# Optimization experiments

Measured on AMD Instinct MI355X. Metric: run time of the kernel, lower is better.

The kernel has to match this reference:

```python
import jax, jax.numpy as jnp
import numpy as np

N_EMBD = 256
BLOCK_SIZE = 128
N_HEAD = 8
HEAD_SIZE = 256
B = 256
T = 128


def setup_inputs() -> dict:
    key = jax.random.key(0)
    ks = jax.random.split(key, 9)
    s = 0.02
    return {
        "x": jax.random.normal(ks[0], (B, T, N_EMBD), dtype=jnp.float32),
        # torch Linear weight layout: [out_features, in_features], stacked over heads
        "Wq": jax.random.normal(ks[1], (N_HEAD, HEAD_SIZE, N_EMBD), dtype=jnp.float32) * s,
        "bq": jax.random.normal(ks[2], (N_HEAD, HEAD_SIZE), dtype=jnp.float32) * s,
        "Wk": jax.random.normal(ks[3], (N_HEAD, HEAD_SIZE, N_EMBD), dtype=jnp.float32) * s,
        "bk": jax.random.normal(ks[4], (N_HEAD, HEAD_SIZE), dtype=jnp.float32) * s,
        "Wv": jax.random.normal(ks[5], (N_HEAD, HEAD_SIZE, N_EMBD), dtype=jnp.float32) * s,
        "bv": jax.random.normal(ks[6], (N_HEAD, HEAD_SIZE), dtype=jnp.float32) * s,
        "Wp": jax.random.normal(ks[7], (N_EMBD, N_EMBD), dtype=jnp.float32) * s,
        "bp": jax.random.normal(ks[8], (N_EMBD,), dtype=jnp.float32) * s,
    }


def reference(x, Wq, bq, Wk, bk, Wv, bv, Wp, bp):
    Bb, Tt, C = x.shape
    scale = C ** (-0.5)  # NOTE: original scales by n_embd (input C), not head_size
    # per-head projections: [h, b, t, d]
    q = jnp.einsum("btc,hdc->hbtd", x, Wq) + bq[:, None, None, :]
    k = jnp.einsum("btc,hdc->hbtd", x, Wk) + bk[:, None, None, :]
    v = jnp.einsum("btc,hdc->hbtd", x, Wv) + bv[:, None, None, :]
    att = jnp.einsum("hbtd,hbsd->hbts", q, k) * scale  # [h,b,t,s]
    causal = jnp.tril(jnp.ones((Tt, Tt), dtype=bool))
    att = jnp.where(causal, att, -jnp.inf)
    att = jax.nn.softmax(att, axis=-1)
    out = jnp.einsum("hbts,hbsd->hbtd", att, v)
    # torch.cat along dim=0 (batch concat, as written in the source)
    out = out.reshape(out.shape[0] * Bb, Tt, out.shape[-1])  # [h*b, t, head_size]
    return out @ Wp.T + bp
```

## Files before the change

### kernel.cpp

```cpp
#include <hip/hip_runtime.h>
#include <hip/hip_bf16.h>
#include <stdint.h>


#define TT 128

typedef __attribute__((ext_vector_type(8))) short short8;
typedef __attribute__((ext_vector_type(4))) float f32x4;

#define WS_X    0u
#define WS_M    16777216u
#define WS_WM   17825792u
#define WS_WB   18874368u
#define WS_BB   18939904u
#define WS_CQ   18948096u

#define LX     0
#define LT     65536
#define LP     65536
#define LH     98304
#define R_UV   131072
#define R_RED  132096
#define LDS_SIZE 134144

#define VMCNT0() asm volatile("s_waitcnt vmcnt(0)" ::: "memory")
#define LGKM0()  asm volatile("s_waitcnt lgkmcnt(0)" ::: "memory")
#define BAR()    do { asm volatile("" ::: "memory"); __builtin_amdgcn_s_barrier(); asm volatile("" ::: "memory"); } while (0)
#define PRIO1()  __builtin_amdgcn_s_setprio(1)
#define PRIO0()  __builtin_amdgcn_s_setprio(0)

typedef __attribute__((address_space(3))) uint32_t lds_u32;
typedef __attribute__((address_space(1))) const uint32_t glb_u32;

__device__ __forceinline__ unsigned short f2bf(float x) {
    union { float f; unsigned u; } v; v.f = x;
    unsigned r = v.u + 0x7FFFu + ((v.u >> 16) & 1u);
    return (unsigned short)(r >> 16);
}
__device__ __forceinline__ unsigned pk2(float a, float b) {
    return (unsigned)f2bf(a) | ((unsigned)f2bf(b) << 16);
}

__global__ __launch_bounds__(256) void convert_pre(
    const float* __restrict__ x,
    const float* __restrict__ Wq, const float* __restrict__ bq,
    const float* __restrict__ Wk, const float* __restrict__ bk,
    const float* __restrict__ Wv, const float* __restrict__ bv,
    const float* __restrict__ Wp, const float* __restrict__ bp,
    char* __restrict__ ws)
{
    extern __shared__ char clds[];
    const int tid = threadIdx.x;
    const int bid = blockIdx.x;

    if (bid < 256) {
        const float* src = x + (size_t)bid * 32768;
        char* dst = ws + WS_X + (size_t)bid * 65536;
        for (int i = tid; i < 8192; i += 256) {
            float4 v = ((const float4*)src)[i];
            int row = i >> 6, c4 = i & 63;
            uint2 u; u.x = pk2(v.x, v.y); u.y = pk2(v.z, v.w);
            *(uint2*)(clds + row * 512 + ((c4 * 8) ^ ((row & 7) << 4))) = u;
        }
        __syncthreads();
        for (int i = tid; i < 4096; i += 256) {
            int l = i & 63, ks = (i >> 6) & 7, g = i >> 9;
            int r = g * 16 + (l & 15);
            int boff = ks * 64 + (l >> 4) * 16;
            uint4 q = *(const uint4*)(clds + r * 512 + (boff ^ ((r & 7) << 4)));
            ((uint4*)dst)[i] = q;
        }
        return;
    }
    if (bid < 384) {
        int id = bid - 256, h = id >> 4, st = id & 15;
        float* wkL = (float*)clds;
        for (int i = tid; i < 4096; i += 256) {
            int d = i >> 4, cc = i & 15;
            wkL[i] = Wk[(size_t)h * 65536 + d * 256 + st * 16 + cc];
        }
        __syncthreads();
        const int c = tid;
        float acc[16];
        #pragma unroll
        for (int j = 0; j < 16; ++j) acc[j] = 0.f;
        #pragma unroll 4
        for (int d = 0; d < 256; ++d) {
            float a = Wq[(size_t)h * 65536 + d * 256 + c];
            #pragma unroll
            for (int j = 0; j < 16; ++j) acc[j] += a * wkL[d * 16 + j];
        }
        char* base = ws + WS_M + (size_t)h * 131072;
        int ks = c >> 5, lgp = (c >> 3) & 3, jb = c & 7;
        #pragma unroll
        for (int j = 0; j < 16; ++j) {
            int cp = st * 16 + j;
            *(unsigned short*)(base + (((st * 8 + ks)) << 10)
                + ((cp & 15) + 16 * lgp) * 16 + jb * 2) = f2bf(acc[j] * 0.0625f);
        }
        return;
    }
    if (bid < 512) {
        int id = bid - 384, h = id >> 4, st = id & 15;
        float* wpL = (float*)clds;
        for (int i = tid; i < 4096; i += 256) {
            int e = i >> 8, d = i & 255;
            wpL[e * 257 + d] = Wp[(size_t)(st * 16 + e) * 256 + d];
        }
        __syncthreads();
        const int c = tid;
        float acc[16];
        #pragma unroll
        for (int j = 0; j < 16; ++j) acc[j] = 0.f;
        #pragma unroll 4
        for (int d = 0; d < 256; ++d) {
            float wv = Wv[(size_t)h * 65536 + d * 256 + c];
            #pragma unroll
            for (int j = 0; j < 16; ++j) acc[j] += wv * wpL[j * 257 + d];
        }
        char* base = ws + WS_WM + (size_t)h * 131072;
        int ks = c >> 5, lgp = (c >> 3) & 3, jb = c & 7;
        #pragma unroll
        for (int j = 0; j < 16; ++j) {
            *(unsigned short*)(base + (((st * 8 + ks)) << 10)
                + (j + 16 * lgp) * 16 + jb * 2) = f2bf(acc[j]);
        }
        return;
    }
    if (bid < 520) {
        const int h = bid - 512;
        {
            uint4 z = {0u,0u,0u,0u};
            for (int i = tid; i < 512; i += 256)
                ((uint4*)(ws + WS_WB + (size_t)h * 8192))[i] = z;
        }
        float* tK = (float*)clds;
        float* tQ = (float*)(clds + 16384);
        const int c = tid;
        float s1 = 0.f, s2 = 0.f;
        for (int d0 = 0; d0 < 256; d0 += 16) {
            __syncthreads();
            for (int i = tid; i < 1024; i += 256) {
                int row = i >> 6, c4 = i & 63;
                ((float4*)tK)[row * 64 + c4] =
                    ((const float4*)(Wk + (size_t)h * 65536 + (size_t)(d0 + row) * 256))[c4];
                ((float4*)tQ)[row * 64 + c4] =
                    ((const float4*)(Wq + (size_t)h * 65536 + (size_t)(d0 + row) * 256))[c4];
            }
            __syncthreads();
            #pragma unroll
            for (int dd = 0; dd < 16; ++dd) {
                s1 += tK[dd * 256 + c] * bq[h * 256 + d0 + dd];
                s2 += tQ[dd * 256 + c] * bk[h * 256 + d0 + dd];
            }
        }
        int ks = c >> 5, lgp = (c >> 3) & 3, jb = c & 7;
        char* base = ws + WS_WB + (size_t)h * 8192 + ks * 1024;
        *(unsigned short*)(base + (0 + 16 * lgp) * 16 + jb * 2) = f2bf(s2 * 0.0625f);
        *(unsigned short*)(base + (1 + 16 * lgp) * 16 + jb * 2) = f2bf(s1 * 0.0625f);
        float* red = (float*)(clds + 32768);
        red[tid] = bq[h * 256 + tid] * bk[h * 256 + tid];
        __syncthreads();
        if (tid == 0) {
            float cq = 0.f;
            for (int d = 0; d < 256; ++d) cq += red[d];
            *(float*)(ws + WS_CQ + h * 4) = cq * 0.0625f;
        }
        return;
    }
    {
        const int st = bid - 520;
        float* wpT = (float*)clds;
        float* bvL = (float*)(clds + 17408);
        for (int i = tid; i < 1024; i += 256) {
            int row = i >> 6, c4 = i & 63;
            float4 v = ((const float4*)(Wp + (size_t)(st * 16 + row) * 256))[c4];
            float* dstp = wpT + row * 257 + c4 * 4;
            dstp[0] = v.x; dstp[1] = v.y; dstp[2] = v.z; dstp[3] = v.w;
        }
        for (int i = tid; i < 512; i += 256)
            ((float4*)bvL)[i] = ((const float4*)bv)[i];
        __syncthreads();
        const int el = tid >> 4, dg = tid & 15;
        #pragma unroll
        for (int h = 0; h < 8; ++h) {
            float p = 0.f;
            #pragma unroll
            for (int dd = 0; dd < 16; ++dd) {
                int d = dg * 16 + dd;
                p += bvL[h * 256 + d] * wpT[el * 257 + d];
            }
            p += __shfl_xor(p, 1);
            p += __shfl_xor(p, 2);
            p += __shfl_xor(p, 4);
            p += __shfl_xor(p, 8);
            if (dg == 0)
                *(float*)(ws + WS_BB + (size_t)h * 1024 + (st * 16 + el) * 4)
                    = bp[st * 16 + el] + p;
        }
        return;
    }
}

__global__ __launch_bounds__(512, 1) void mha_fused(
    const char* __restrict__ ws, float* __restrict__ out)
{
    extern __shared__ char lds[];
    const int tid = threadIdx.x;
    const int w  = tid >> 6, l = tid & 63;
    const int lg = l >> 4, lr = l & 15;
    const int mq = w & 3, nh = w >> 2;
    const int bid = blockIdx.x;
    const int xcd = bid & 7, j = bid >> 3;
    const int h = j & 7;
    const int b = ((j >> 3) << 3) | xcd;
    const size_t orow = ((size_t)(h * 256 + b)) * TT;

    const char* Xf  = ws + WS_X  + (size_t)b * 65536;
    const char* Mh  = ws + WS_M  + (size_t)h * 131072;
    const char* WMh = ws + WS_WM + (size_t)h * 131072;
    const char* WBh = ws + WS_WB + (size_t)h * 8192;

    {
        const char* src = Xf + tid * 16;
        #pragma unroll
        for (int p = 0; p < 8; ++p)
            __builtin_amdgcn_global_load_lds((glb_u32*)(src + p * 8192),
                (lds_u32*)(lds + LX + tid * 16 + p * 8192), 16, 0, 0);
    }
    VMCNT0(); BAR();

    {
        f32x4 vacc[2] = {f32x4{0.f,0.f,0.f,0.f}, f32x4{0.f,0.f,0.f,0.f}};
        #pragma unroll
        for (int ks = 0; ks < 8; ++ks) {
            short8 wb  = *(const short8*)(WBh + (ks << 10) + l*16);
            short8 xa0 = *(const short8*)(lds + LX + (((mq*2 + 0)*8 + ks) << 10) + l*16);
            short8 xa1 = *(const short8*)(lds + LX + (((mq*2 + 1)*8 + ks) << 10) + l*16);
            vacc[0] = __builtin_amdgcn_mfma_f32_16x16x32_bf16(xa0, wb, vacc[0], 0, 0, 0);
            vacc[1] = __builtin_amdgcn_mfma_f32_16x16x32_bf16(xa1, wb, vacc[1], 0, 0, 0);
        }
        if (nh == 0 && lr < 2) {
            #pragma unroll
            for (int mt = 0; mt < 2; ++mt)
                #pragma unroll
                for (int r = 0; r < 4; ++r) {
                    int t = mq*32 + mt*16 + lg*4 + r;
                    *(float*)(lds + R_UV + lr*512 + t*4) = vacc[mt][r];
                }
        }
    }

    #pragma unroll
    for (int pass = 0; pass < 2; ++pass) {
        const int ga = w*2 + pass;
        f32x4 acc[8];
        #pragma unroll
        for (int i = 0; i < 8; ++i) acc[i] = f32x4{0.f,0.f,0.f,0.f};
        #pragma unroll
        for (int ks = 0; ks < 8; ++ks) {
            short8 nb = *(const short8*)(Mh + (((ga*8 + ks)) << 10) + l*16);
            PRIO1();
            #pragma unroll
            for (int mt = 0; mt < 8; ++mt) {
                short8 xa = *(const short8*)(lds + LX + (((mt*8 + ks)) << 10) + l*16);
                acc[mt] = __builtin_amdgcn_mfma_f32_16x16x32_bf16(xa, nb, acc[mt], 0, 0, 0);
            }
            PRIO0();
        }
        #pragma unroll
        for (int mt = 0; mt < 8; ++mt)
            #pragma unroll
            for (int r = 0; r < 4; ++r) {
                int t = mt*16 + lg*4 + r;
                int c = ga*16 + lr;
                *(unsigned short*)(lds + LT + t*512 + ((c*2) ^ ((t&7)<<4)))
                    = f2bf(acc[mt][r]);
            }
    }
    LGKM0(); BAR();

    f32x4 sacc[2][4];
    #pragma unroll
    for (int i = 0; i < 2; ++i)
        #pragma unroll
        for (int jj = 0; jj < 4; ++jj) sacc[i][jj] = f32x4{0.f,0.f,0.f,0.f};
    #pragma unroll
    for (int ks2 = 0; ks2 < 8; ++ks2) {
        short8 ta[2];
        #pragma unroll
        for (int mt = 0; mt < 2; ++mt) {
            int t2 = mq*32 + mt*16 + lr;
            ta[mt] = *(const short8*)(lds + LT + t2*512 + ((ks2*64 + lg*16) ^ ((t2&7)<<4)));
        }
        short8 sb[4];
        #pragma unroll
        for (int nt = 0; nt < 4; ++nt)
            sb[nt] = *(const short8*)(lds + LX + (((nh*4+nt)*8 + ks2) << 10) + l*16);
        PRIO1();
        #pragma unroll
        for (int mt = 0; mt < 2; ++mt)
            #pragma unroll
            for (int nt = 0; nt < 4; ++nt)
                sacc[mt][nt] = __builtin_amdgcn_mfma_f32_16x16x32_bf16(ta[mt], sb[nt], sacc[mt][nt], 0, 0, 0);
        PRIO0();
    }

    {
        const float cq = *(const float*)(ws + WS_CQ + h*4);
        float uu[4];
        #pragma unroll
        for (int nt = 0; nt < 4; ++nt)
            uu[nt] = *(const float*)(lds + R_UV + 512 + (nh*64 + nt*16 + lr)*4);
        float* redM = (float*)(lds + R_RED);
        float* redS = redM + 256;
        float rmax[2][4];
        #pragma unroll
        for (int mt = 0; mt < 2; ++mt)
            #pragma unroll
            for (int r = 0; r < 4; ++r) {
                int t = mq*32 + mt*16 + lg*4 + r;
                float vt = *(const float*)(lds + R_UV + t*4) + cq;
                float m = -1e30f;
                #pragma unroll
                for (int nt = 0; nt < 4; ++nt) {
                    int s = nh*64 + nt*16 + lr;
                    float sv = sacc[mt][nt][r] + vt + uu[nt];
                    if (s > t) sv = -1e30f;
                    sacc[mt][nt][r] = sv;
                    m = fmaxf(m, sv);
                }
                m = fmaxf(m, __shfl_xor(m, 1));
                m = fmaxf(m, __shfl_xor(m, 2));
                m = fmaxf(m, __shfl_xor(m, 4));
                m = fmaxf(m, __shfl_xor(m, 8));
                rmax[mt][r] = m;
            }
        if (lr == 0) {
            #pragma unroll
            for (int mt = 0; mt < 2; ++mt)
                #pragma unroll
                for (int r = 0; r < 4; ++r)
                    redM[nh*128 + mq*32 + mt*16 + lg*4 + r] = rmax[mt][r];
        }
        LGKM0(); BAR();
        float rsum[2][4];
        #pragma unroll
        for (int mt = 0; mt < 2; ++mt)
            #pragma unroll
            for (int r = 0; r < 4; ++r) {
                int t = mq*32 + mt*16 + lg*4 + r;
                float m = fmaxf(redM[t], redM[128 + t]);
                float ssum = 0.f;
                #pragma unroll
                for (int nt = 0; nt < 4; ++nt) {
                    float p = __expf(sacc[mt][nt][r] - m);
                    sacc[mt][nt][r] = p;
                    ssum += p;
                }
                ssum += __shfl_xor(ssum, 1);
                ssum += __shfl_xor(ssum, 2);
                ssum += __shfl_xor(ssum, 4);
                ssum += __shfl_xor(ssum, 8);
                rsum[mt][r] = ssum;
            }
        if (lr == 0) {
            #pragma unroll
            for (int mt = 0; mt < 2; ++mt)
                #pragma unroll
                for (int r = 0; r < 4; ++r)
                    redS[nh*128 + mq*32 + mt*16 + lg*4 + r] = rsum[mt][r];
        }
        LGKM0(); BAR();
        #pragma unroll
        for (int mt = 0; mt < 2; ++mt)
            #pragma unroll
            for (int r = 0; r < 4; ++r) {
                int t = mq*32 + mt*16 + lg*4 + r;
                float inv = 1.0f / (redS[t] + redS[128 + t]);
                #pragma unroll
                for (int nt = 0; nt < 4; ++nt) {
                    int s = nh*64 + nt*16 + lr;
                    *(unsigned short*)(lds + LP + t*256 + ((s*2) ^ ((t&7)<<4)))
                        = f2bf(sacc[mt][nt][r] * inv);
                }
            }
    }
    LGKM0(); BAR();

    short8 pa[2][4];
    #pragma unroll
    for (int mt = 0; mt < 2; ++mt) {
        int t2 = mq*32 + mt*16 + lr;
        #pragma unroll
        for (int ks = 0; ks < 4; ++ks)
            pa[mt][ks] = *(const short8*)(lds + LP + t2*256 + ((ks*64 + lg*16) ^ ((t2&7)<<4)));
    }

    const float* bbp = (const float*)(ws + WS_BB + h*1024);
    #pragma unroll
    for (int eh = 0; eh < 2; ++eh) {
        {
            f32x4 acc[8];
            #pragma unroll
            for (int i = 0; i < 8; ++i) acc[i] = f32x4{0.f,0.f,0.f,0.f};
            #pragma unroll
            for (int ks = 0; ks < 8; ++ks) {
                short8 wa = *(const short8*)(WMh + ((((eh*8 + w)*8 + ks)) << 10) + l*16);
                PRIO1();
                #pragma unroll
                for (int nt = 0; nt < 8; ++nt) {
                    short8 sb = *(const short8*)(lds + LX + (((nt*8 + ks)) << 10) + l*16);
                    acc[nt] = __builtin_amdgcn_mfma_f32_16x16x32_bf16(wa, sb, acc[nt], 0, 0, 0);
                }
                PRIO0();
            }
            #pragma unroll
            for (int nt = 0; nt < 8; ++nt)
                #pragma unroll
                for (int r = 0; r < 4; ++r) {
                    int el = w*16 + lg*4 + r;
                    int s  = nt*16 + lr;
                    *(unsigned short*)(lds + LH + el*256 + ((s*2) ^ ((el&7)<<4)))
                        = f2bf(acc[nt][r]);
                }
        }
        LGKM0(); BAR();
        #pragma unroll
        for (int ec = 0; ec < 2; ++ec) {
            f32x4 acc[2][2];
            #pragma unroll
            for (int i = 0; i < 2; ++i)
                #pragma unroll
                for (int jj = 0; jj < 2; ++jj) acc[i][jj] = f32x4{0.f,0.f,0.f,0.f};
            #pragma unroll
            for (int ks = 0; ks < 4; ++ks) {
                short8 hb[2];
                #pragma unroll
                for (int nt = 0; nt < 2; ++nt) {
                    int erl = (nh*4 + ec*2 + nt)*16 + lr;
                    hb[nt] = *(const short8*)(lds + LH + erl*256 + ((ks*64 + lg*16) ^ ((erl&7)<<4)));
                }
                PRIO1();
                #pragma unroll
                for (int mt = 0; mt < 2; ++mt)
                    #pragma unroll
                    for (int nt = 0; nt < 2; ++nt)
                        acc[mt][nt] = __builtin_amdgcn_mfma_f32_16x16x32_bf16(pa[mt][ks], hb[nt], acc[mt][nt], 0, 0, 0);
                PRIO0();
            }
            #pragma unroll
            for (int nt = 0; nt < 2; ++nt) {
                int e = eh*128 + (nh*4 + ec*2 + nt)*16 + lr;
                float bbv = bbp[e];
                #pragma unroll
                for (int mt = 0; mt < 2; ++mt)
                    #pragma unroll
                    for (int r = 0; r < 4; ++r) {
                        int t = mq*32 + mt*16 + lg*4 + r;
                        out[(orow + t) * 256 + e] = acc[mt][nt][r] + bbv;
                    }
            }
        }
        if (eh == 0) { LGKM0(); BAR(); }
    }
}

extern "C" void kernel_launch(void* const* d_in, const int* in_sizes, int n_in,
                              void* d_out, int out_size, void* d_ws, size_t ws_size,
                              hipStream_t stream) {
    (void)in_sizes; (void)n_in; (void)out_size; (void)ws_size;
    const float* x  = (const float*)d_in[0];
    const float* Wq = (const float*)d_in[1];
    const float* bq = (const float*)d_in[2];
    const float* Wk = (const float*)d_in[3];
    const float* bk = (const float*)d_in[4];
    const float* Wv = (const float*)d_in[5];
    const float* bv = (const float*)d_in[6];
    const float* Wp = (const float*)d_in[7];
    const float* bp = (const float*)d_in[8];
    char* ws = (char*)d_ws;

    hipFuncSetAttribute((const void*)convert_pre,
                        hipFuncAttributeMaxDynamicSharedMemorySize, 65536);
    convert_pre<<<dim3(536), dim3(256), 65536, stream>>>(
        x, Wq, bq, Wk, bk, Wv, bv, Wp, bp, ws);

    hipFuncSetAttribute((const void*)mha_fused,
                        hipFuncAttributeMaxDynamicSharedMemorySize, LDS_SIZE);
    mha_fused<<<dim3(2048), dim3(512), LDS_SIZE, stream>>>(ws, (float*)d_out);
}
```

Before: 267.2 us.

## Double workgroup to 1024 threads and repartition all GEMM stages across 16 waves

The fused attention kernel now runs 16 waves per block instead of 8, and every stage is repartitioned to match: the projection, scores, softmax, H and output GEMMs each handle half the tiles per wave. The goal is more latency hiding and more in-flight MFMA work per CU, since only one block of about 131 KB LDS fits per CU. The cost is more waves contending for the same LDS and barriers, less register reuse of loaded fragments per wave, and tighter register limits at 1024 threads.

```diff
diff --git a/kernel.cpp b/kernel.cpp
--- a/kernel.cpp
+++ b/kernel.cpp
@@ -202,14 +202,14 @@
     }
 }
 
-__global__ __launch_bounds__(512, 1) void mha_fused(
+__global__ __launch_bounds__(1024, 1) void mha_fused(
     const char* __restrict__ ws, float* __restrict__ out)
 {
     extern __shared__ char lds[];
     const int tid = threadIdx.x;
     const int w  = tid >> 6, l = tid & 63;
     const int lg = l >> 4, lr = l & 15;
-    const int mq = w & 3, nh = w >> 2;
+    const int mq = w & 7, nh = w >> 3;
     const int bid = blockIdx.x;
     const int xcd = bid & 7, j = bid >> 3;
     const int h = j & 7;
@@ -224,42 +224,36 @@
     {
         const char* src = Xf + tid * 16;
         #pragma unroll
-        for (int p = 0; p < 8; ++p)
-            __builtin_amdgcn_global_load_lds((glb_u32*)(src + p * 8192),
-                (lds_u32*)(lds + LX + tid * 16 + p * 8192), 16, 0, 0);
+        for (int p = 0; p < 4; ++p)
+            __builtin_amdgcn_global_load_lds((glb_u32*)(src + p * 16384),
+                (lds_u32*)(lds + LX + tid * 16 + p * 16384), 16, 0, 0);
     }
     VMCNT0(); BAR();
 
+    if (nh == 0) {
+        f32x4 vacc = f32x4{0.f,0.f,0.f,0.f};
+        #pragma unroll
+        for (int ks = 0; ks < 8; ++ks) {
+            short8 wb = *(const short8*)(WBh + (ks << 10) + l*16);
+            short8 xa = *(const short8*)(lds + LX + (((mq*8 + ks)) << 10) + l*16);
+            vacc = __builtin_amdgcn_mfma_f32_16x16x32_bf16(xa, wb, vacc, 0, 0, 0);
+        }
+        if (lr < 2) {
+            #pragma unroll
+            for (int r = 0; r < 4; ++r) {
+                int t = mq*16 + lg*4 + r;
+                *(float*)(lds + R_UV + lr*512 + t*4) = vacc[r];
+            }
+        }
+    }
+
     {
-        f32x4 vacc[2] = {f32x4{0.f,0.f,0.f,0.f}, f32x4{0.f,0.f,0.f,0.f}};
+        f32x4 acc[8];
+        #pragma unroll
+        for (int i = 0; i < 8; ++i) acc[i] = f32x4{0.f,0.f,0.f,0.f};
         #pragma unroll
         for (int ks = 0; ks < 8; ++ks) {
-            short8 wb  = *(const short8*)(WBh + (ks << 10) + l*16);
-            short8 xa0 = *(const short8*)(lds + LX + (((mq*2 + 0)*8 + ks) << 10) + l*16);
-            short8 xa1 = *(const short8*)(lds + LX + (((mq*2 + 1)*8 + ks) << 10) + l*16);
-            vacc[0] = __builtin_amdgcn_mfma_f32_16x16x32_bf16(xa0, wb, vacc[0], 0, 0, 0);
-            vacc[1] = __builtin_amdgcn_mfma_f32_16x16x32_bf16(xa1, wb, vacc[1], 0, 0, 0);
-        }
-        if (nh == 0 && lr < 2) {
-            #pragma unroll
-            for (int mt = 0; mt < 2; ++mt)
-                #pragma unroll
-                for (int r = 0; r < 4; ++r) {
-                    int t = mq*32 + mt*16 + lg*4 + r;
-                    *(float*)(lds + R_UV + lr*512 + t*4) = vacc[mt][r];
-                }
-        }
-    }
-
-    #pragma unroll
-    for (int pass = 0; pass < 2; ++pass) {
-        const int ga = w*2 + pass;
-        f32x4 acc[8];
-        #pragma unroll
-        for (int i = 0; i < 8; ++i) acc[i] = f32x4{0.f,0.f,0.f,0.f};
-        #pragma unroll
-        for (int ks = 0; ks < 8; ++ks) {
-            short8 nb = *(const short8*)(Mh + (((ga*8 + ks)) << 10) + l*16);
+            short8 nb = *(const short8*)(Mh + (((w*8 + ks)) << 10) + l*16);
             PRIO1();
             #pragma unroll
             for (int mt = 0; mt < 8; ++mt) {
@@ -273,36 +267,28 @@
             #pragma unroll
             for (int r = 0; r < 4; ++r) {
                 int t = mt*16 + lg*4 + r;
-                int c = ga*16 + lr;
+                int c = w*16 + lr;
                 *(unsigned short*)(lds + LT + t*512 + ((c*2) ^ ((t&7)<<4)))
                     = f2bf(acc[mt][r]);
             }
     }
     LGKM0(); BAR();
 
-    f32x4 sacc[2][4];
+    f32x4 sacc[4];
     #pragma unroll
-    for (int i = 0; i < 2; ++i)
-        #pragma unroll
-        for (int jj = 0; jj < 4; ++jj) sacc[i][jj] = f32x4{0.f,0.f,0.f,0.f};
+    for (int i = 0; i < 4; ++i) sacc[i] = f32x4{0.f,0.f,0.f,0.f};
     #pragma unroll
     for (int ks2 = 0; ks2 < 8; ++ks2) {
-        short8 ta[2];
-        #pragma unroll
-        for (int mt = 0; mt < 2; ++mt) {
-            int t2 = mq*32 + mt*16 + lr;
-            ta[mt] = *(const short8*)(lds + LT + t2*512 + ((ks2*64 + lg*16) ^ ((t2&7)<<4)));
-        }
+        int t2 = mq*16 + lr;
+        short8 ta = *(const short8*)(lds + LT + t2*512 + ((ks2*64 + lg*16) ^ ((t2&7)<<4)));
         short8 sb[4];
         #pragma unroll
         for (int nt = 0; nt < 4; ++nt)
             sb[nt] = *(const short8*)(lds + LX + (((nh*4+nt)*8 + ks2) << 10) + l*16);
         PRIO1();
         #pragma unroll
-        for (int mt = 0; mt < 2; ++mt)
-            #pragma unroll
-            for (int nt = 0; nt < 4; ++nt)
-                sacc[mt][nt] = __builtin_amdgcn_mfma_f32_16x16x32_bf16(ta[mt], sb[nt], sacc[mt][nt], 0, 0, 0);
+        for (int nt = 0; nt < 4; ++nt)
+            sacc[nt] = __builtin_amdgcn_mfma_f32_16x16x32_bf16(ta, sb[nt], sacc[nt], 0, 0, 0);
         PRIO0();
     }
 
@@ -314,113 +300,102 @@
             uu[nt] = *(const float*)(lds + R_UV + 512 + (nh*64 + nt*16 + lr)*4);
         float* redM = (float*)(lds + R_RED);
         float* redS = redM + 256;
-        float rmax[2][4];
-        #pragma unroll
-        for (int mt = 0; mt < 2; ++mt)
-            #pragma unroll
-            for (int r = 0; r < 4; ++r) {
-                int t = mq*32 + mt*16 + lg*4 + r;
-                float vt = *(const float*)(lds + R_UV + t*4) + cq;
-                float m = -1e30f;
-                #pragma unroll
-                for (int nt = 0; nt < 4; ++nt) {
-                    int s = nh*64 + nt*16 + lr;
-                    float sv = sacc[mt][nt][r] + vt + uu[nt];
-                    if (s > t) sv = -1e30f;
-                    sacc[mt][nt][r] = sv;
-                    m = fmaxf(m, sv);
-                }
-                m = fmaxf(m, __shfl_xor(m, 1));
-                m = fmaxf(m, __shfl_xor(m, 2));
-                m = fmaxf(m, __shfl_xor(m, 4));
-                m = fmaxf(m, __shfl_xor(m, 8));
-                rmax[mt][r] = m;
-            }
+        float rmax[4];
+        #pragma unroll
+        for (int r = 0; r < 4; ++r) {
+            int t = mq*16 + lg*4 + r;
+            float vt = *(const float*)(lds + R_UV + t*4) + cq;
+            float m = -1e30f;
+            #pragma unroll
+            for (int nt = 0; nt < 4; ++nt) {
+                int s = nh*64 + nt*16 + lr;
+                float sv = sacc[nt][r] + vt + uu[nt];
+                if (s > t) sv = -1e30f;
+                sacc[nt][r] = sv;
+                m = fmaxf(m, sv);
+            }
+            m = fmaxf(m, __shfl_xor(m, 1));
+            m = fmaxf(m, __shfl_xor(m, 2));
+            m = fmaxf(m, __shfl_xor(m, 4));
+            m = fmaxf(m, __shfl_xor(m, 8));
+            rmax[r] = m;
+        }
         if (lr == 0) {
             #pragma unroll
-            for (int mt = 0; mt < 2; ++mt)
-                #pragma unroll
-                for (int r = 0; r < 4; ++r)
-                    redM[nh*128 + mq*32 + mt*16 + lg*4 + r] = rmax[mt][r];
+            for (int r = 0; r < 4; ++r)
+                redM[nh*128 + mq*16 + lg*4 + r] = rmax[r];
         }
         LGKM0(); BAR();
-        float rsum[2][4];
-        #pragma unroll
-        for (int mt = 0; mt < 2; ++mt)
-            #pragma unroll
-            for (int r = 0; r < 4; ++r) {
-                int t = mq*32 + mt*16 + lg*4 + r;
-                float m = fmaxf(redM[t], redM[128 + t]);
-                float ssum = 0.f;
-                #pragma unroll
-                for (int nt = 0; nt < 4; ++nt) {
-                    float p = __expf(sacc[mt][nt][r] - m);
-                    sacc[mt][nt][r] = p;
-                    ssum += p;
-                }
-                ssum += __shfl_xor(ssum, 1);
-                ssum += __shfl_xor(ssum, 2);
-                ssum += __shfl_xor(ssum, 4);
-                ssum += __shfl_xor(ssum, 8);
-                rsum[mt][r] = ssum;
-            }
+        float rsum[4];
+        #pragma unroll
+        for (int r = 0; r < 4; ++r) {
+            int t = mq*16 + lg*4 + r;
+            float m = fmaxf(redM[t], redM[128 + t]);
+            float ssum = 0.f;
+            #pragma unroll
+            for (int nt = 0; nt < 4; ++nt) {
+                float p = __expf(sacc[nt][r] - m);
+                sacc[nt][r] = p;
+                ssum += p;
+            }
+            ssum += __shfl_xor(ssum, 1);
+            ssum += __shfl_xor(ssum, 2);
+            ssum += __shfl_xor(ssum, 4);
+            ssum += __shfl_xor(ssum, 8);
+            rsum[r] = ssum;
+        }
         if (lr == 0) {
             #pragma unroll
-            for (int mt = 0; mt < 2; ++mt)
-                #pragma unroll
-                for (int r = 0; r < 4; ++r)
-                    redS[nh*128 + mq*32 + mt*16 + lg*4 + r] = rsum[mt][r];
+            for (int r = 0; r < 4; ++r)
+                redS[nh*128 + mq*16 + lg*4 + r] = rsum[r];
         }
         LGKM0(); BAR();
         #pragma unroll
-        for (int mt = 0; mt < 2; ++mt)
-            #pragma unroll
-            for (int r = 0; r < 4; ++r) {
-                int t = mq*32 + mt*16 + lg*4 + r;
-                float inv = 1.0f / (redS[t] + redS[128 + t]);
-                #pragma unroll
-                for (int nt = 0; nt < 4; ++nt) {
-                    int s = nh*64 + nt*16 + lr;
-                    *(unsigned short*)(lds + LP + t*256 + ((s*2) ^ ((t&7)<<4)))
-                        = f2bf(sacc[mt][nt][r] * inv);
-                }
-            }
+        for (int r = 0; r < 4; ++r) {
+            int t = mq*16 + lg*4 + r;
+            float inv = 1.0f / (redS[t] + redS[128 + t]);
+            #pragma unroll
+            for (int nt = 0; nt < 4; ++nt) {
+                int s = nh*64 + nt*16 + lr;
+                *(unsigned short*)(lds + LP + t*256 + ((s*2) ^ ((t&7)<<4)))
+                    = f2bf(sacc[nt][r] * inv);
+            }
+        }
     }
     LGKM0(); BAR();
 
-    short8 pa[2][4];
-    #pragma unroll
-    for (int mt = 0; mt < 2; ++mt) {
-        int t2 = mq*32 + mt*16 + lr;
+    short8 pa[4];
+    {
+        int t2 = mq*16 + lr;
         #pragma unroll
         for (int ks = 0; ks < 4; ++ks)
-            pa[mt][ks] = *(const short8*)(lds + LP + t2*256 + ((ks*64 + lg*16) ^ ((t2&7)<<4)));
+            pa[ks] = *(const short8*)(lds + LP + t2*256 + ((ks*64 + lg*16) ^ ((t2&7)<<4)));
     }
 
     const float* bbp = (const float*)(ws + WS_BB + h*1024);
     #pragma unroll
     for (int eh = 0; eh < 2; ++eh) {
         {
-            f32x4 acc[8];
-            #pragma unroll
-            for (int i = 0; i < 8; ++i) acc[i] = f32x4{0.f,0.f,0.f,0.f};
+            f32x4 acc[4];
+            #pragma unroll
+            for (int i = 0; i < 4; ++i) acc[i] = f32x4{0.f,0.f,0.f,0.f};
             #pragma unroll
             for (int ks = 0; ks < 8; ++ks) {
-                short8 wa = *(const short8*)(WMh + ((((eh*8 + w)*8 + ks)) << 10) + l*16);
+                short8 wa = *(const short8*)(WMh + ((((eh*8 + mq)*8 + ks)) << 10) + l*16);
                 PRIO1();
                 #pragma unroll
-                for (int nt = 0; nt < 8; ++nt) {
-                    short8 sb = *(const short8*)(lds + LX + (((nt*8 + ks)) << 10) + l*16);
+                for (int nt = 0; nt < 4; ++nt) {
+                    short8 sb = *(const short8*)(lds + LX + ((((nh*4+nt)*8 + ks)) << 10) + l*16);
                     acc[nt] = __builtin_amdgcn_mfma_f32_16x16x32_bf16(wa, sb, acc[nt], 0, 0, 0);
                 }
                 PRIO0();
             }
             #pragma unroll
-            for (int nt = 0; nt < 8; ++nt)
+            for (int nt = 0; nt < 4; ++nt)
                 #pragma unroll
                 for (int r = 0; r < 4; ++r) {
-                    int el = w*16 + lg*4 + r;
-                    int s  = nt*16 + lr;
+                    int el = mq*16 + lg*4 + r;
+                    int s  = (nh*4+nt)*16 + lr;
                     *(unsigned short*)(lds + LH + el*256 + ((s*2) ^ ((el&7)<<4)))
                         = f2bf(acc[nt][r]);
                 }
@@ -428,38 +403,32 @@
         LGKM0(); BAR();
         #pragma unroll
         for (int ec = 0; ec < 2; ++ec) {
-            f32x4 acc[2][2];
-            #pragma unroll
-            for (int i = 0; i < 2; ++i)
-                #pragma unroll
-                for (int jj = 0; jj < 2; ++jj) acc[i][jj] = f32x4{0.f,0.f,0.f,0.f};
+            f32x4 acc[2];
+            acc[0] = f32x4{0.f,0.f,0.f,0.f};
+            acc[1] = f32x4{0.f,0.f,0.f,0.f};
             #pragma unroll
             for (int ks = 0; ks < 4; ++ks) {
                 short8 hb[2];
                 #pragma unroll
                 for (int nt = 0; nt < 2; ++nt) {
-                    int erl = (nh*4 + ec*2 + nt)*16 + lr;
+                    int erl = nh*64 + (ec*2 + nt)*16 + lr;
                     hb[nt] = *(const short8*)(lds + LH + erl*256 + ((ks*64 + lg*16) ^ ((erl&7)<<4)));
                 }
                 PRIO1();
                 #pragma unroll
-                for (int mt = 0; mt < 2; ++mt)
-                    #pragma unroll
-                    for (int nt = 0; nt < 2; ++nt)
-                        acc[mt][nt] = __builtin_amdgcn_mfma_f32_16x16x32_bf16(pa[mt][ks], hb[nt], acc[mt][nt], 0, 0, 0);
+                for (int nt = 0; nt < 2; ++nt)
+                    acc[nt] = __builtin_amdgcn_mfma_f32_16x16x32_bf16(pa[ks], hb[nt], acc[nt], 0, 0, 0);
                 PRIO0();
             }
             #pragma unroll
             for (int nt = 0; nt < 2; ++nt) {
-                int e = eh*128 + (nh*4 + ec*2 + nt)*16 + lr;
+                int e = eh*128 + nh*64 + (ec*2 + nt)*16 + lr;
                 float bbv = bbp[e];
                 #pragma unroll
-                for (int mt = 0; mt < 2; ++mt)
-                    #pragma unroll
-                    for (int r = 0; r < 4; ++r) {
-                        int t = mq*32 + mt*16 + lg*4 + r;
-                        out[(orow + t) * 256 + e] = acc[mt][nt][r] + bbv;
-                    }
+                for (int r = 0; r < 4; ++r) {
+                    int t = mq*16 + lg*4 + r;
+                    out[(orow + t) * 256 + e] = acc[nt][r] + bbv;
+                }
             }
         }
         if (eh == 0) { LGKM0(); BAR(); }
@@ -488,5 +457,5 @@
 
     hipFuncSetAttribute((const void*)mha_fused,
                         hipFuncAttributeMaxDynamicSharedMemorySize, LDS_SIZE);
-    mha_fused<<<dim3(2048), dim3(512), LDS_SIZE, stream>>>(ws, (float*)d_out);
+    mha_fused<<<dim3(2048), dim3(1024), LDS_SIZE, stream>>>(ws, (float*)d_out);
 }
```

After: 239.0 us. 1.12x faster.
